# Kernel tuning notes

Measured on AMD Instinct MI355X. Metric: run time of the kernel, lower is better.

## Reference

```python
import jax, jax.numpy as jnp
import numpy as np

N, E, IN_F, EDGE_F, HID, S = 200000, 600000, 28, 4, 128, 20000
NUM_LAYERS = 4
L = NUM_LAYERS - 1
BN_EPS = 1e-5


def setup_inputs() -> dict:
    key = jax.random.key(0)
    ks = jax.random.split(key, 20)
    p = lambda k, shape: (jax.random.normal(k, shape, dtype=jnp.float32) * 0.1)
    return {
        'x': jax.random.normal(ks[0], (N, IN_F), dtype=jnp.float32),
        'edge_index': jax.random.randint(ks[1], (2, E), 0, N),
        'edge_attr': jax.random.normal(ks[2], (E, EDGE_F), dtype=jnp.float32),
        'edge_weight': jax.random.uniform(ks[3], (E,), dtype=jnp.float32),
        'node_mask': (jax.random.uniform(ks[4], (N,)) > 0.5).astype(jnp.float32),
        'subgraphs2nodes': jax.random.randint(ks[5], (N,), 0, S),
        # layer-1 params (in_features -> hidden)
        'be1_W1': p(ks[6], (EDGE_F, IN_F)), 'be1_b1': jnp.zeros((IN_F,), jnp.float32),
        'be1_W2': p(ks[7], (IN_F, IN_F)), 'be1_b2': jnp.zeros((IN_F,), jnp.float32),
        'm1_W1': p(ks[8], (IN_F, HID)), 'm1_b1': jnp.zeros((HID,), jnp.float32),
        'm1_W2': p(ks[9], (HID, HID)), 'm1_b2': jnp.zeros((HID,), jnp.float32),
        'bn1_g': jnp.ones((HID,), jnp.float32), 'bn1_b': jnp.zeros((HID,), jnp.float32),
        'eps1': jnp.zeros((), jnp.float32),
        # layers 2..NUM_LAYERS, stacked (hidden -> hidden)
        'beW1': p(ks[10], (L, EDGE_F, HID)), 'beb1': jnp.zeros((L, HID), jnp.float32),
        'beW2': p(ks[11], (L, HID, HID)), 'beb2': jnp.zeros((L, HID), jnp.float32),
        'mW1': p(ks[12], (L, HID, HID)), 'mb1': jnp.zeros((L, HID), jnp.float32),
        'mW2': p(ks[13], (L, HID, HID)), 'mb2': jnp.zeros((L, HID), jnp.float32),
        'bng': jnp.ones((L, HID), jnp.float32), 'bnb': jnp.zeros((L, HID), jnp.float32),
        'eps': jnp.zeros((L,), jnp.float32),
    }


def _mlp2(h, W1, b1, W2, b2):
    # Linear -> ReLU -> Linear
    return jnp.dot(jax.nn.relu(jnp.dot(h, W1) + b1), W2) + b2


def _gine(x, src, dst, edge_attr, edge_weight, eps,
          beW1, beb1, beW2, beb2, W1, b1, W2, b2, g, beta):
    # bond encoder on edge features
    e = _mlp2(edge_attr, beW1, beb1, beW2, beb2)            # [E, d]
    # message: relu(x_j + e_ij) * w_ij, aggregated at dst via scatter-add
    m = jax.nn.relu(x[src] + e) * edge_weight[:, None]      # [E, d]
    aggr = jax.ops.segment_sum(m, dst, num_segments=N)      # [N, d]
    h = (1.0 + eps) * x + aggr
    # node MLP: Linear,ReLU,Linear,BN(train mode),ReLU
    h = _mlp2(h, W1, b1, W2, b2)
    mu = jnp.mean(h, axis=0)
    var = jnp.mean((h - mu) ** 2, axis=0)
    h = (h - mu) * jax.lax.rsqrt(var + BN_EPS) * g + beta
    return jax.nn.relu(h)


def reference(x, edge_index, edge_attr, edge_weight, node_mask, subgraphs2nodes,
              be1_W1, be1_b1, be1_W2, be1_b2, m1_W1, m1_b1, m1_W2, m1_b2,
              bn1_g, bn1_b, eps1,
              beW1, beb1, beW2, beb2, mW1, mb1, mW2, mb2, bng, bnb, eps):
    src, dst = edge_index[0], edge_index[1]
    h = _gine(x, src, dst, edge_attr, edge_weight, eps1,
              be1_W1, be1_b1, be1_W2, be1_b2,
              m1_W1, m1_b1, m1_W2, m1_b2, bn1_g, bn1_b)
    for i in range(L):
        h_new = _gine(h, src, dst, edge_attr, edge_weight, eps[i],
                      beW1[i], beb1[i], beW2[i], beb2[i],
                      mW1[i], mb1[i], mW2[i], mb2[i], bng[i], bnb[i])
        h = h + h_new  # residual
    # float node_mask branch + global_add_pool over subgraphs2nodes
    h = h * node_mask[:, None]
    return jax.ops.segment_sum(h, subgraphs2nodes, num_segments=S)  # [S, HID]
```

## Files before the change

### kernel.cpp

```cpp
#include <hip/hip_runtime.h>
#include <hip/hip_bf16.h>


#define BNEPS 1e-5f
#define LDA 136
#define SCAN_NB 240

typedef __attribute__((ext_vector_type(8))) short bf16x8;
typedef __attribute__((ext_vector_type(8))) unsigned short u16x8;
typedef __attribute__((ext_vector_type(4))) float f32x4;

__device__ inline short f2bf(float f) {
    __hip_bfloat16 h = __float2bfloat16(f);
    return *reinterpret_cast<short*>(&h);
}
__device__ inline unsigned short f2bfu(float f) {
    __hip_bfloat16 h = __float2bfloat16(f);
    return *reinterpret_cast<unsigned short*>(&h);
}
__device__ inline float bf2f(unsigned short u) {
    union { unsigned int i; float f; } v; v.i = ((unsigned int)u) << 16; return v.f;
}


__global__ __launch_bounds__(256) void k_prep(
    const float* __restrict__ m1W2, const float* __restrict__ beW2,
    const float* __restrict__ mW1, const float* __restrict__ mW2,
    short* __restrict__ out)
{
    __shared__ float tileS[64][65];
    int b = blockIdx.x, mat = b >> 2, t = b & 3;
    const float* Wsrc;
    if (mat == 0) Wsrc = m1W2;
    else {
        int l = (mat - 1) / 3, which = (mat - 1) % 3;
        Wsrc = (which == 0) ? beW2 + (size_t)l * 16384
             : (which == 1) ? mW1 + (size_t)l * 16384
             :                mW2 + (size_t)l * 16384;
    }
    short* dst = out + (size_t)mat * 16384;
    int tr = (t >> 1) * 64, tc = (t & 1) * 64;
    for (int i = threadIdx.x; i < 4096; i += 256) {
        int r = i >> 6, c = i & 63;
        tileS[r][c] = Wsrc[(size_t)(tr + r) * 128 + (tc + c)];
    }
    __syncthreads();
    for (int i = threadIdx.x; i < 4096; i += 256) {
        int kl = i & 63, nl = i >> 6;
        int n = tc + nl, k = tr + kl;
        int fo = (((n >> 4) * 4 + (k >> 5)) * 64 + (((k >> 3) & 3) * 16 + (n & 15))) * 8 + (k & 7);
        dst[fo] = f2bf(tileS[kl][nl]);
    }
}

__global__ __launch_bounds__(256) void k_prep1(
    const float* __restrict__ W1, short* __restrict__ out)
{
    for (int i = threadIdx.x; i < 4096; i += 256) {
        int j = i & 7, sub = (i >> 3) & 63, nt = i >> 9;
        int quad = sub >> 4, l15 = sub & 15;
        int n = nt * 16 + l15, k = quad * 8 + j;
        out[i] = (k < 28) ? f2bf(W1[(size_t)k * 128 + n]) : (short)0;
    }
}

__global__ __launch_bounds__(256) void k_prep28(
    const float* __restrict__ W2, short* __restrict__ out)
{
    for (int i = threadIdx.x; i < 32 * 32; i += 256) {
        int n = i >> 5, k = i & 31;
        out[i] = (n < 28 && k < 28) ? f2bf(W2[(size_t)k * 28 + n]) : (short)0;
    }
}

__global__ __launch_bounds__(256) void k_prepx(
    const float* __restrict__ x, unsigned short* __restrict__ xbf, int N)
{
    int total = N * 32;
    for (int i = blockIdx.x * 256 + threadIdx.x; i < total; i += gridDim.x * 256) {
        int n = i >> 5, c = i & 31;
        xbf[i] = (c < 28) ? f2bfu(x[(size_t)n * 28 + c]) : (unsigned short)0;
    }
}

__global__ __launch_bounds__(256) void k_count(
    const int* __restrict__ ei, int* __restrict__ counts, int E)
{
    for (int e = blockIdx.x * 256 + threadIdx.x; e < E; e += gridDim.x * 256)
        atomicAdd(&counts[ei[E + e]], 1);
}

__global__ __launch_bounds__(256) void k_count2(
    const int* __restrict__ s2n, const float* __restrict__ mask,
    int* __restrict__ counts2, int N)
{
    for (int n = blockIdx.x * 256 + threadIdx.x; n < N; n += gridDim.x * 256)
        if (mask[n] != 0.f) atomicAdd(&counts2[s2n[n]], 1);
}

__global__ __launch_bounds__(256) void k_scanA(
    const int* __restrict__ counts, int* __restrict__ bsum, int N, int seg)
{
    __shared__ int red[256];
    int b = blockIdx.x;
    int lo = b * seg, hi = min(lo + seg, N);
    int s = 0;
    for (int i = lo + threadIdx.x; i < hi; i += 256) s += counts[i];
    red[threadIdx.x] = s;
    __syncthreads();
    for (int d = 128; d > 0; d >>= 1) {
        if (threadIdx.x < d) red[threadIdx.x] += red[threadIdx.x + d];
        __syncthreads();
    }
    if (threadIdx.x == 0) bsum[b] = red[0];
}

__global__ __launch_bounds__(256) void k_scanB(
    int* __restrict__ bsum, int nb, int* __restrict__ offs, int N)
{
    __shared__ int sh[256];
    int v = (threadIdx.x < nb) ? bsum[threadIdx.x] : 0;
    sh[threadIdx.x] = v;
    __syncthreads();
    for (int d = 1; d < 256; d <<= 1) {
        int t = (threadIdx.x >= d) ? sh[threadIdx.x - d] : 0;
        __syncthreads();
        sh[threadIdx.x] += t;
        __syncthreads();
    }
    if (threadIdx.x < nb) bsum[threadIdx.x] = sh[threadIdx.x] - v;
    if (threadIdx.x == 0) offs[N] = sh[255];
}

__global__ __launch_bounds__(256) void k_scanC(
    const int* __restrict__ counts, const int* __restrict__ bsum,
    int* __restrict__ offs, int* __restrict__ cursor, int N, int seg)
{
    __shared__ int sh[256];
    int b = blockIdx.x;
    int lo = b * seg, hi = min(lo + seg, N);
    int base = bsum[b];
    for (int t0 = lo; t0 < hi; t0 += 256) {
        int i = t0 + threadIdx.x;
        int v = (i < hi) ? counts[i] : 0;
        sh[threadIdx.x] = v;
        __syncthreads();
        for (int d = 1; d < 256; d <<= 1) {
            int t = (threadIdx.x >= d) ? sh[threadIdx.x - d] : 0;
            __syncthreads();
            sh[threadIdx.x] += t;
            __syncthreads();
        }
        int excl = base + sh[threadIdx.x] - v;
        if (i < hi) { offs[i] = excl; cursor[i] = excl; }
        int tileTotal = sh[255];
        __syncthreads();
        base += tileTotal;
    }
}

__global__ __launch_bounds__(256) void k_scatter(
    const int* __restrict__ ei, const float* __restrict__ ew,
    const float4* __restrict__ ea4,
    int* __restrict__ cursor, int2* __restrict__ pmeta,
    float4* __restrict__ pea4, int E)
{
    for (int e = blockIdx.x * 256 + threadIdx.x; e < E; e += gridDim.x * 256) {
        int d = ei[E + e];
        int pos = atomicAdd(&cursor[d], 1);
        pmeta[pos] = make_int2(ei[e], __float_as_int(ew[e]));
        pea4[pos] = ea4[e];
    }
}

__global__ __launch_bounds__(256) void k_scatter2(
    const int* __restrict__ s2n, const float* __restrict__ mask,
    int* __restrict__ cursor2, int* __restrict__ perm2, int N)
{
    for (int n = blockIdx.x * 256 + threadIdx.x; n < N; n += gridDim.x * 256)
        if (mask[n] != 0.f) {
            int pos = atomicAdd(&cursor2[s2n[n]], 1);
            perm2[pos] = n;
        }
}

__global__ __launch_bounds__(256, 3) void k_emsg(
    const float4* __restrict__ pea4,
    const float* __restrict__ W1, const float* __restrict__ b1,
    const short* __restrict__ W2f, const float* __restrict__ b2,
    unsigned short* __restrict__ emsg, const int* __restrict__ offs,
    int n0, int n1)
{
    __shared__ short As[64 * LDA];
    __shared__ short Bs[16384];
    int e0 = offs[n0], e1 = offs[n1];
    int tid = threadIdx.x;
    int w = tid >> 6, lane = tid & 63;
    int l15 = lane & 15, quad = lane >> 4;
    int rb = w * 16;
    for (int i = tid; i < 2048; i += 256)
        *(bf16x8*)&Bs[i * 8] = *(const bf16x8*)&W2f[i * 8];
    int c2 = lane * 2;
    float w1a[4], w1b[4];
    #pragma unroll
    for (int a = 0; a < 4; ++a) { w1a[a] = W1[a * 128 + c2]; w1b[a] = W1[a * 128 + c2 + 1]; }
    float b1a = b1[c2], b1b = b1[c2 + 1];
    float b2r[8];
    #pragma unroll
    for (int nt = 0; nt < 8; ++nt) b2r[nt] = b2[nt * 16 + l15];
    __syncthreads();

    const float* peaf = (const float*)pea4;
    int numTiles = (e1 - e0 + 63) >> 6;
    for (int tile = blockIdx.x; tile < numTiles; tile += gridDim.x) {
        int base = e0 + tile * 64;
        int eidx = base + rb + (lane >> 2);
        float v = (eidx < e1) ? peaf[(size_t)(base + rb) * 4 + lane] : 0.f;
        #pragma unroll
        for (int e = 0; e < 16; ++e) {
            float a0v = __shfl(v, e * 4 + 0);
            float a1v = __shfl(v, e * 4 + 1);
            float a2v = __shfl(v, e * 4 + 2);
            float a3v = __shfl(v, e * 4 + 3);
            float t0 = fmaf(a0v, w1a[0], fmaf(a1v, w1a[1], fmaf(a2v, w1a[2], fmaf(a3v, w1a[3], b1a))));
            float t1 = fmaf(a0v, w1b[0], fmaf(a1v, w1b[1], fmaf(a2v, w1b[2], fmaf(a3v, w1b[3], b1b))));
            unsigned int pk = ((unsigned int)f2bfu(fmaxf(t1, 0.f)) << 16) | f2bfu(fmaxf(t0, 0.f));
            *(unsigned int*)&As[(rb + e) * LDA + c2] = pk;
        }
        f32x4 acc[8];
        #pragma unroll
        for (int nt = 0; nt < 8; ++nt) acc[nt] = (f32x4){0.f, 0.f, 0.f, 0.f};
        #pragma unroll
        for (int kt = 0; kt < 4; ++kt) {
            bf16x8 af = *(bf16x8*)&As[(rb + l15) * LDA + kt * 32 + quad * 8];
            #pragma unroll
            for (int nt = 0; nt < 8; ++nt) {
                bf16x8 bf = *(const bf16x8*)&Bs[((nt * 4 + kt) * 64 + lane) * 8];
                acc[nt] = __builtin_amdgcn_mfma_f32_16x16x32_bf16(af, bf, acc[nt], 0, 0, 0);
            }
        }
        #pragma unroll
        for (int nt = 0; nt < 8; ++nt) {
            #pragma unroll
            for (int r = 0; r < 4; ++r)
                As[(rb + quad * 4 + r) * LDA + nt * 16 + l15] = f2bf(acc[nt][r] + b2r[nt]);
        }
        #pragma unroll
        for (int it = 0; it < 4; ++it) {
            int arow = rb + it * 4 + quad;
            int gr = base + arow;
            if (gr < e1)
                *(bf16x8*)&emsg[(size_t)(gr - e0) * 128 + l15 * 8] = *(bf16x8*)&As[arow * LDA + l15 * 8];
        }
    }
}

__global__ __launch_bounds__(256) void k_emsg28_mm(
    const float4* __restrict__ pea4,
    const float* __restrict__ W1, const float* __restrict__ b1,
    const short* __restrict__ W2t28,
    const float* __restrict__ b2,
    unsigned short* __restrict__ emsg28, int E)
{
    __shared__ short Bs[32 * 40];
    __shared__ short As[64 * 40];
    __shared__ float eas[64][4];
    __shared__ float b2s[32];
    int tid = threadIdx.x;
    for (int i = tid; i < 32 * 32; i += 256) {
        int n = i >> 5, k = i & 31;
        Bs[n * 40 + k] = W2t28[i];
    }
    if (tid < 32) b2s[tid] = (tid < 28) ? b2[tid] : 0.f;
    int j = tid & 31, sub = tid >> 5;
    float w10 = 0.f, w11 = 0.f, w12 = 0.f, w13 = 0.f, b1j = 0.f;
    if (j < 28) { w10 = W1[j]; w11 = W1[28 + j]; w12 = W1[56 + j]; w13 = W1[84 + j]; b1j = b1[j]; }
    int w = tid >> 6, lane = tid & 63;
    int l15 = lane & 15, quad = lane >> 4;
    __syncthreads();

    int numTiles = (E + 63) >> 6;
    for (int tile = blockIdx.x; tile < numTiles; tile += gridDim.x) {
        int base = tile * 64;
        __syncthreads();
        if (tid < 64) {
            int k = base + tid;
            float4 a = (k < E) ? pea4[k] : make_float4(0.f, 0.f, 0.f, 0.f);
            eas[tid][0] = a.x; eas[tid][1] = a.y; eas[tid][2] = a.z; eas[tid][3] = a.w;
        }
        __syncthreads();
        #pragma unroll
        for (int q = 0; q < 8; ++q) {
            int e = q * 8 + sub;
            float t = fmaf(eas[e][0], w10, fmaf(eas[e][1], w11,
                      fmaf(eas[e][2], w12, fmaf(eas[e][3], w13, b1j))));
            As[e * 40 + j] = (j < 28) ? f2bf(fmaxf(t, 0.f)) : (short)0;
        }
        __syncthreads();
        f32x4 acc[2];
        acc[0] = (f32x4){0.f, 0.f, 0.f, 0.f};
        acc[1] = (f32x4){0.f, 0.f, 0.f, 0.f};
        bf16x8 af = *(bf16x8*)&As[(w * 16 + l15) * 40 + quad * 8];
        #pragma unroll
        for (int nt = 0; nt < 2; ++nt) {
            bf16x8 bf = *(bf16x8*)&Bs[(nt * 16 + l15) * 40 + quad * 8];
            acc[nt] = __builtin_amdgcn_mfma_f32_16x16x32_bf16(af, bf, acc[nt], 0, 0, 0);
        }
        __syncthreads();
        #pragma unroll
        for (int nt = 0; nt < 2; ++nt) {
            int col = nt * 16 + l15;
            float bb = b2s[col];
            #pragma unroll
            for (int r = 0; r < 4; ++r)
                As[(w * 16 + quad * 4 + r) * 40 + col] = f2bf(acc[nt][r] + bb);
        }
        __syncthreads();
        for (int i = tid; i < 64 * 28; i += 256) {
            int row = i / 28, col = i - row * 28;
            int gr = base + row;
            if (gr < E) emsg28[(size_t)gr * 28 + col] = As[row * 40 + col];
        }
    }
}

__global__ __launch_bounds__(256) void k_gather(
    const unsigned short* __restrict__ h, const int* __restrict__ offs,
    const int2* __restrict__ pmeta, const unsigned short* __restrict__ emsg,
    unsigned short* __restrict__ a0,
    const float* __restrict__ epsp, int epsIdx,
    int n0, int n1)
{
    int grp = threadIdx.x >> 5, lane = threadIdx.x & 31;
    int n = n0 + blockIdx.x * 8 + grp;
    if (n >= n1) return;
    int e0 = offs[n0];
    int k0 = offs[n], k1 = offs[n + 1];
    float s = 1.0f + epsp[epsIdx];
    ushort4 hv0 = *(const ushort4*)&h[(size_t)n * 128 + lane * 4];
    float m0 = s * bf2f(hv0.x), m1 = s * bf2f(hv0.y);
    float m2 = s * bf2f(hv0.z), m3 = s * bf2f(hv0.w);
    int2 mtA = make_int2(0, 0), mtB = make_int2(0, 0);
    int2 mtC = make_int2(0, 0), mtD = make_int2(0, 0);
    ushort4 evA = {0,0,0,0}, hvA = {0,0,0,0}, evB = {0,0,0,0}, hvB = {0,0,0,0};
    ushort4 evC = {0,0,0,0}, hvC = {0,0,0,0}, evD = {0,0,0,0}, hvD = {0,0,0,0};
    #define GLOADSLOT(mt, ev, hv, kk) \
        if ((kk) < k1) { \
            mt = pmeta[kk]; \
            ev = *(const ushort4*)&emsg[(size_t)((kk) - e0) * 128 + lane * 4]; \
            hv = *(const ushort4*)&h[(size_t)mt.x * 128 + lane * 4]; \
        }
    GLOADSLOT(mtA, evA, hvA, k0)
    GLOADSLOT(mtB, evB, hvB, k0 + 1)
    GLOADSLOT(mtC, evC, hvC, k0 + 2)
    GLOADSLOT(mtD, evD, hvD, k0 + 3)
    for (int k = k0; k < k1; ++k) {
        float w = __int_as_float(mtA.y);
        m0 += fmaxf(bf2f(hvA.x) + bf2f(evA.x), 0.f) * w;
        m1 += fmaxf(bf2f(hvA.y) + bf2f(evA.y), 0.f) * w;
        m2 += fmaxf(bf2f(hvA.z) + bf2f(evA.z), 0.f) * w;
        m3 += fmaxf(bf2f(hvA.w) + bf2f(evA.w), 0.f) * w;
        mtA = mtB; evA = evB; hvA = hvB;
        mtB = mtC; evB = evC; hvB = hvC;
        mtC = mtD; evC = evD; hvC = hvD;
        GLOADSLOT(mtD, evD, hvD, k + 4)
    }
    #undef GLOADSLOT
    ushort4 o;
    o.x = f2bfu(m0); o.y = f2bfu(m1); o.z = f2bfu(m2); o.w = f2bfu(m3);
    *(ushort4*)&a0[(size_t)n * 128 + lane * 4] = o;
}

__global__ __launch_bounds__(256) void k_gather28(
    const float* __restrict__ x, const unsigned short* __restrict__ xbf,
    const int* __restrict__ offs,
    const int2* __restrict__ pmeta, const unsigned short* __restrict__ emsg28,
    const float* __restrict__ eps1, float* __restrict__ u28, int N)
{
    int grp = threadIdx.x >> 5, lane = threadIdx.x & 31;
    int n = blockIdx.x * 8 + grp;
    if (n >= N || lane >= 28) return;
    float s = 1.0f + eps1[0];
    int k0 = offs[n], k1 = offs[n + 1];
    float m = 0.f;
    int2 mtA = make_int2(0, 0), mtB = make_int2(0, 0);
    int2 mtC = make_int2(0, 0), mtD = make_int2(0, 0);
    unsigned short eA = 0, xA = 0, eB = 0, xB = 0;
    unsigned short eC = 0, xC = 0, eD = 0, xD = 0;
    #define GLOADSLOT28(mt, ee, xx, kk) \
        if ((kk) < k1) { \
            mt = pmeta[kk]; \
            ee = emsg28[(size_t)(kk) * 28 + lane]; \
            xx = xbf[(size_t)mt.x * 32 + lane]; \
        }
    GLOADSLOT28(mtA, eA, xA, k0)
    GLOADSLOT28(mtB, eB, xB, k0 + 1)
    GLOADSLOT28(mtC, eC, xC, k0 + 2)
    GLOADSLOT28(mtD, eD, xD, k0 + 3)
    for (int k = k0; k < k1; ++k) {
        float w = __int_as_float(mtA.y);
        m += fmaxf(bf2f(xA) + bf2f(eA), 0.f) * w;
        mtA = mtB; eA = eB; xA = xB;
        mtB = mtC; eB = eC; xB = xC;
        mtC = mtD; eC = eD; xC = xD;
        GLOADSLOT28(mtD, eD, xD, k + 4)
    }
    #undef GLOADSLOT28
    u28[(size_t)n * 28 + lane] = fmaf(s, x[(size_t)n * 28 + lane], m);
}

__global__ __launch_bounds__(512, 2) void k_mlp(
    const unsigned short* __restrict__ src, const short* __restrict__ W1f,
    const float* __restrict__ b1, const short* __restrict__ W2f,
    const float* __restrict__ b2, unsigned short* __restrict__ dst,
    float* __restrict__ stats, int N)
{
    __shared__ short As[256 * LDA];
    __shared__ short Bs1[16384];
    __shared__ short Bs2[16384];
    __shared__ float sstat[256];
    int tid = threadIdx.x;
    for (int i = tid; i < 2048; i += 512) {
        *(bf16x8*)&Bs1[i * 8] = *(const bf16x8*)&W1f[i * 8];
        *(bf16x8*)&Bs2[i * 8] = *(const bf16x8*)&W2f[i * 8];
    }
    if (tid < 256) sstat[tid] = 0.f;
    int w = tid >> 6, lane = tid & 63;
    int l15 = lane & 15, quad = lane >> 4;
    int rb = w * 32;
    float b1r[8], b2r[8], lsum[8], lsq[8];
    #pragma unroll
    for (int nt = 0; nt < 8; ++nt) {
        b1r[nt] = b1[nt * 16 + l15]; b2r[nt] = b2[nt * 16 + l15];
        lsum[nt] = 0.f; lsq[nt] = 0.f;
    }
    int numTiles = (N + 255) >> 8;
    bf16x8 st[8];
    {
        int tile = blockIdx.x;
        if (tile < numTiles) {
            int base = tile * 256;
            #pragma unroll
            for (int kk = 0; kk < 8; ++kk) {
                int i = tid + kk * 512;
                int rr = base + (i >> 4);
                st[kk] = (rr < N) ? *(const bf16x8*)&src[(size_t)rr * 128 + (i & 15) * 8]
                                  : (bf16x8){0, 0, 0, 0, 0, 0, 0, 0};
            }
        }
    }
    __syncthreads();

    for (int tile = blockIdx.x; tile < numTiles; tile += gridDim.x) {
        int base = tile * 256;
        #pragma unroll
        for (int kk = 0; kk < 8; ++kk) {
            int i = tid + kk * 512;
            *(bf16x8*)&As[(i >> 4) * LDA + (i & 15) * 8] = st[kk];
        }
        int tnext = tile + gridDim.x;
        if (tnext < numTiles) {
            int bn = tnext * 256;
            #pragma unroll
            for (int kk = 0; kk < 8; ++kk) {
                int i = tid + kk * 512;
                int rr = bn + (i >> 4);
                st[kk] = (rr < N) ? *(const bf16x8*)&src[(size_t)rr * 128 + (i & 15) * 8]
                                  : (bf16x8){0, 0, 0, 0, 0, 0, 0, 0};
            }
        }
        __syncthreads();
        f32x4 acc[2][8];
        #pragma unroll
        for (int rg = 0; rg < 2; ++rg)
            #pragma unroll
            for (int nt = 0; nt < 8; ++nt) acc[rg][nt] = (f32x4){0.f, 0.f, 0.f, 0.f};
        #pragma unroll
        for (int kt = 0; kt < 4; ++kt) {
            bf16x8 af0 = *(bf16x8*)&As[(rb + l15) * LDA + kt * 32 + quad * 8];
            bf16x8 af1 = *(bf16x8*)&As[(rb + 16 + l15) * LDA + kt * 32 + quad * 8];
            #pragma unroll
            for (int nt = 0; nt < 8; ++nt) {
                bf16x8 bf = *(const bf16x8*)&Bs1[((nt * 4 + kt) * 64 + lane) * 8];
                acc[0][nt] = __builtin_amdgcn_mfma_f32_16x16x32_bf16(af0, bf, acc[0][nt], 0, 0, 0);
                acc[1][nt] = __builtin_amdgcn_mfma_f32_16x16x32_bf16(af1, bf, acc[1][nt], 0, 0, 0);
            }
        }
        #pragma unroll
        for (int rg = 0; rg < 2; ++rg)
            #pragma unroll
            for (int nt = 0; nt < 8; ++nt)
                #pragma unroll
                for (int r = 0; r < 4; ++r)
                    As[(rb + rg * 16 + quad * 4 + r) * LDA + nt * 16 + l15] =
                        f2bf(fmaxf(acc[rg][nt][r] + b1r[nt], 0.f));
        #pragma unroll
        for (int rg = 0; rg < 2; ++rg)
            #pragma unroll
            for (int nt = 0; nt < 8; ++nt) acc[rg][nt] = (f32x4){0.f, 0.f, 0.f, 0.f};
        #pragma unroll
        for (int kt = 0; kt < 4; ++kt) {
            bf16x8 af0 = *(bf16x8*)&As[(rb + l15) * LDA + kt * 32 + quad * 8];
            bf16x8 af1 = *(bf16x8*)&As[(rb + 16 + l15) * LDA + kt * 32 + quad * 8];
            #pragma unroll
            for (int nt = 0; nt < 8; ++nt) {
                bf16x8 bf = *(const bf16x8*)&Bs2[((nt * 4 + kt) * 64 + lane) * 8];
                acc[0][nt] = __builtin_amdgcn_mfma_f32_16x16x32_bf16(af0, bf, acc[0][nt], 0, 0, 0);
                acc[1][nt] = __builtin_amdgcn_mfma_f32_16x16x32_bf16(af1, bf, acc[1][nt], 0, 0, 0);
            }
        }
        #pragma unroll
        for (int rg = 0; rg < 2; ++rg)
            #pragma unroll
            for (int nt = 0; nt < 8; ++nt) {
                int row0 = base + rb + rg * 16 + quad * 4;
                #pragma unroll
                for (int r = 0; r < 4; ++r) {
                    float z = acc[rg][nt][r] + b2r[nt];
                    if (row0 + r < N) { lsum[nt] += z; lsq[nt] = fmaf(z, z, lsq[nt]); }
                    As[(rb + rg * 16 + quad * 4 + r) * LDA + nt * 16 + l15] = f2bf(z);
                }
            }
        #pragma unroll
        for (int it = 0; it < 8; ++it) {
            int arow = rb + it * 4 + quad;
            int rr = base + arow;
            if (rr < N)
                *(bf16x8*)&dst[(size_t)rr * 128 + l15 * 8] = *(bf16x8*)&As[arow * LDA + l15 * 8];
        }
        __syncthreads();
    }
    #pragma unroll
    for (int nt = 0; nt < 8; ++nt) {
        atomicAdd(&sstat[nt * 16 + l15], lsum[nt]);
        atomicAdd(&sstat[128 + nt * 16 + l15], lsq[nt]);
    }
    __syncthreads();
    if (tid < 256) atomicAdd(&stats[tid], sstat[tid]);
}

__global__ __launch_bounds__(512, 2) void k_mlp1(
    const float* __restrict__ u28, const short* __restrict__ W1f,
    const float* __restrict__ b1, const short* __restrict__ W2f,
    const float* __restrict__ b2, unsigned short* __restrict__ dst,
    float* __restrict__ stats, int N)
{
    __shared__ short A28[256 * 40];
    __shared__ short As[256 * LDA];
    __shared__ short Bs1[4096];
    __shared__ short Bs2[16384];
    __shared__ float sstat[256];
    int tid = threadIdx.x;
    if (tid < 512) {
        int i = tid;
        *(bf16x8*)&Bs1[i * 8] = *(const bf16x8*)&W1f[i * 8];
    }
    for (int i = tid; i < 2048; i += 512)
        *(bf16x8*)&Bs2[i * 8] = *(const bf16x8*)&W2f[i * 8];
    for (int i = tid; i < 1024; i += 512) {
        int row = i >> 2, c = 28 + (i & 3);
        A28[row * 40 + c] = 0;
    }
    if (tid < 256) sstat[tid] = 0.f;
    int w = tid >> 6, lane = tid & 63;
    int l15 = lane & 15, quad = lane >> 4;
    int rb = w * 32;
    float b1r[8], b2r[8], lsum[8], lsq[8];
    #pragma unroll
    for (int nt = 0; nt < 8; ++nt) {
        b1r[nt] = b1[nt * 16 + l15]; b2r[nt] = b2[nt * 16 + l15];
        lsum[nt] = 0.f; lsq[nt] = 0.f;
    }
    int numTiles = (N + 255) >> 8;
    float stf[14];
    {
        int tile = blockIdx.x;
        if (tile < numTiles) {
            int base = tile * 256;
            #pragma unroll
            for (int kk = 0; kk < 14; ++kk) {
                int idx = tid + kk * 512;
                int row = idx / 28, col = idx - row * 28;
                int rr = base + row;
                stf[kk] = (rr < N) ? u28[(size_t)rr * 28 + col] : 0.f;
            }
        }
    }
    __syncthreads();

    for (int tile = blockIdx.x; tile < numTiles; tile += gridDim.x) {
        int base = tile * 256;
        #pragma unroll
        for (int kk = 0; kk < 14; ++kk) {
            int idx = tid + kk * 512;
            int row = idx / 28, col = idx - row * 28;
            A28[row * 40 + col] = f2bf(stf[kk]);
        }
        int tnext = tile + gridDim.x;
        if (tnext < numTiles) {
            int bn = tnext * 256;
            #pragma unroll
            for (int kk = 0; kk < 14; ++kk) {
                int idx = tid + kk * 512;
                int row = idx / 28, col = idx - row * 28;
                int rr = bn + row;
                stf[kk] = (rr < N) ? u28[(size_t)rr * 28 + col] : 0.f;
            }
        }
        __syncthreads();
        f32x4 acc[2][8];
        #pragma unroll
        for (int rg = 0; rg < 2; ++rg)
            #pragma unroll
            for (int nt = 0; nt < 8; ++nt) acc[rg][nt] = (f32x4){0.f, 0.f, 0.f, 0.f};
        {
            bf16x8 af0 = *(bf16x8*)&A28[(rb + l15) * 40 + quad * 8];
            bf16x8 af1 = *(bf16x8*)&A28[(rb + 16 + l15) * 40 + quad * 8];
            #pragma unroll
            for (int nt = 0; nt < 8; ++nt) {
                bf16x8 bf = *(const bf16x8*)&Bs1[(nt * 64 + lane) * 8];
                acc[0][nt] = __builtin_amdgcn_mfma_f32_16x16x32_bf16(af0, bf, acc[0][nt], 0, 0, 0);
                acc[1][nt] = __builtin_amdgcn_mfma_f32_16x16x32_bf16(af1, bf, acc[1][nt], 0, 0, 0);
            }
        }
        #pragma unroll
        for (int rg = 0; rg < 2; ++rg)
            #pragma unroll
            for (int nt = 0; nt < 8; ++nt)
                #pragma unroll
                for (int r = 0; r < 4; ++r)
                    As[(rb + rg * 16 + quad * 4 + r) * LDA + nt * 16 + l15] =
                        f2bf(fmaxf(acc[rg][nt][r] + b1r[nt], 0.f));
        __syncthreads();
        #pragma unroll
        for (int rg = 0; rg < 2; ++rg)
            #pragma unroll
            for (int nt = 0; nt < 8; ++nt) acc[rg][nt] = (f32x4){0.f, 0.f, 0.f, 0.f};
        #pragma unroll
        for (int kt = 0; kt < 4; ++kt) {
            bf16x8 af0 = *(bf16x8*)&As[(rb + l15) * LDA + kt * 32 + quad * 8];
            bf16x8 af1 = *(bf16x8*)&As[(rb + 16 + l15) * LDA + kt * 32 + quad * 8];
            #pragma unroll
            for (int nt = 0; nt < 8; ++nt) {
                bf16x8 bf = *(const bf16x8*)&Bs2[((nt * 4 + kt) * 64 + lane) * 8];
                acc[0][nt] = __builtin_amdgcn_mfma_f32_16x16x32_bf16(af0, bf, acc[0][nt], 0, 0, 0);
                acc[1][nt] = __builtin_amdgcn_mfma_f32_16x16x32_bf16(af1, bf, acc[1][nt], 0, 0, 0);
            }
        }
        #pragma unroll
        for (int rg = 0; rg < 2; ++rg)
            #pragma unroll
            for (int nt = 0; nt < 8; ++nt) {
                int row0 = base + rb + rg * 16 + quad * 4;
                #pragma unroll
                for (int r = 0; r < 4; ++r) {
                    float z = acc[rg][nt][r] + b2r[nt];
                    if (row0 + r < N) { lsum[nt] += z; lsq[nt] = fmaf(z, z, lsq[nt]); }
                    As[(rb + rg * 16 + quad * 4 + r) * LDA + nt * 16 + l15] = f2bf(z);
                }
            }
        #pragma unroll
        for (int it = 0; it < 8; ++it) {
            int arow = rb + it * 4 + quad;
            int rr = base + arow;
            if (rr < N)
                *(bf16x8*)&dst[(size_t)rr * 128 + l15 * 8] = *(bf16x8*)&As[arow * LDA + l15 * 8];
        }
        __syncthreads();
    }
    #pragma unroll
    for (int nt = 0; nt < 8; ++nt) {
        atomicAdd(&sstat[nt * 16 + l15], lsum[nt]);
        atomicAdd(&sstat[128 + nt * 16 + l15], lsq[nt]);
    }
    __syncthreads();
    if (tid < 256) atomicAdd(&stats[tid], sstat[tid]);
}

__global__ __launch_bounds__(256) void k_bn(
    const unsigned short* __restrict__ z, const float* __restrict__ stats,
    const float* __restrict__ g, const float* __restrict__ bb, float invN,
    unsigned short* __restrict__ h, int residual, int N)
{
    __shared__ float ss[256];
    if (threadIdx.x < 128) {
        int j = threadIdx.x;
        float mu  = stats[j] * invN;
        float var = fmaf(stats[128 + j], invN, -mu * mu);
        float sc  = rsqrtf(fmaxf(var, 0.f) + BNEPS) * g[j];
        ss[j] = sc;
        ss[128 + j] = fmaf(-mu, sc, bb[j]);
    }
    __syncthreads();
    int idx8 = blockIdx.x * 256 + threadIdx.x;
    int stride = gridDim.x * 256;
    int c0 = (idx8 & 15) * 8;
    float scl[8], sht[8];
    #pragma unroll
    for (int r = 0; r < 8; ++r) { scl[r] = ss[c0 + r]; sht[r] = ss[128 + c0 + r]; }
    int total8 = N * 16;
    for (; idx8 < total8; idx8 += stride) {
        int n = idx8 >> 4;
        u16x8 z8 = *(const u16x8*)&z[(size_t)n * 128 + c0];
        float hn[8];
        #pragma unroll
        for (int r = 0; r < 8; ++r)
            hn[r] = fmaxf(fmaf(bf2f(z8[r]), scl[r], sht[r]), 0.f);
        if (residual) {
            u16x8 h8 = *(const u16x8*)&h[(size_t)n * 128 + c0];
            #pragma unroll
            for (int r = 0; r < 8; ++r) hn[r] += bf2f(h8[r]);
        }
        u16x8 o;
        #pragma unroll
        for (int r = 0; r < 8; ++r) o[r] = f2bfu(hn[r]);
        *(u16x8*)&h[(size_t)n * 128 + c0] = o;
    }
}

__global__ __launch_bounds__(256) void k_poolbn(
    const unsigned short* __restrict__ z, const unsigned short* __restrict__ hprev,
    const float* __restrict__ stats, const float* __restrict__ g,
    const float* __restrict__ bb, float invN,
    const int* __restrict__ offs2, const int* __restrict__ perm2,
    float* __restrict__ out, int S)
{
    __shared__ float ss[256];
    if (threadIdx.x < 128) {
        int j = threadIdx.x;
        float mu  = stats[j] * invN;
        float var = fmaf(stats[128 + j], invN, -mu * mu);
        float sc  = rsqrtf(fmaxf(var, 0.f) + BNEPS) * g[j];
        ss[j] = sc;
        ss[128 + j] = fmaf(-mu, sc, bb[j]);
    }
    __syncthreads();
    int w = threadIdx.x >> 6, lane = threadIdx.x & 63;
    int s = blockIdx.x * 4 + w;
    if (s >= S) return;
    int c0 = lane * 2;
    float scl0 = ss[c0], scl1 = ss[c0 + 1];
    float sht0 = ss[128 + c0], sht1 = ss[128 + c0 + 1];
    int k0 = offs2[s], k1 = offs2[s + 1];
    float a0 = 0.f, a1 = 0.f;
    for (int k = k0; k < k1; ++k) {
        int n = perm2[k];
        ushort2 zv = *(const ushort2*)&z[(size_t)n * 128 + c0];
        ushort2 hv = *(const ushort2*)&hprev[(size_t)n * 128 + c0];
        a0 += fmaxf(fmaf(bf2f(zv.x), scl0, sht0), 0.f) + bf2f(hv.x);
        a1 += fmaxf(fmaf(bf2f(zv.y), scl1, sht1), 0.f) + bf2f(hv.y);
    }
    *(float2*)&out[(size_t)s * 128 + c0] = make_float2(a0, a1);
}

extern "C" void kernel_launch(void* const* d_in, const int* in_sizes, int n_in,
                              void* d_out, int out_size, void* d_ws, size_t ws_size,
                              hipStream_t stream) {
    const float* x    = (const float*)d_in[0];
    const int*   ei   = (const int*)d_in[1];
    const float* ea   = (const float*)d_in[2];
    const float* ew   = (const float*)d_in[3];
    const float* mask = (const float*)d_in[4];
    const int*   s2n  = (const int*)d_in[5];
    const float* be1W1 = (const float*)d_in[6];
    const float* be1b1 = (const float*)d_in[7];
    const float* be1W2 = (const float*)d_in[8];
    const float* be1b2 = (const float*)d_in[9];
    const float* m1W1  = (const float*)d_in[10];
    const float* m1b1  = (const float*)d_in[11];
    const float* m1W2  = (const float*)d_in[12];
    const float* m1b2  = (const float*)d_in[13];
    const float* bn1g  = (const float*)d_in[14];
    const float* bn1b  = (const float*)d_in[15];
    const float* eps1  = (const float*)d_in[16];
    const float* beW1  = (const float*)d_in[17];
    const float* beb1  = (const float*)d_in[18];
    const float* beW2  = (const float*)d_in[19];
    const float* beb2  = (const float*)d_in[20];
    const float* mW1   = (const float*)d_in[21];
    const float* mb1   = (const float*)d_in[22];
    const float* mW2   = (const float*)d_in[23];
    const float* mb2   = (const float*)d_in[24];
    const float* bng   = (const float*)d_in[25];
    const float* bnb   = (const float*)d_in[26];
    const float* epsL  = (const float*)d_in[27];

    const int N = in_sizes[0] / 28;
    const int E = in_sizes[1] / 2;
    const int S = out_size / 128;
    const float invN = 1.0f / (float)N;
    const int NS = N / 2;
    const int EMC = E / 2 + 8192;

    auto al16 = [](size_t v) { return (v + 15) & ~(size_t)15; };
    char* ws = (char*)d_ws;
    size_t offH      = 0;
    size_t offA0     = al16(offH + (size_t)N * 256);
    size_t offEm     = al16(offA0 + (size_t)N * 256);
    size_t emBytes   = (size_t)EMC * 256;
    if ((size_t)E * 56 > emBytes) emBytes = (size_t)E * 56;
    size_t offStats  = al16(offEm + emBytes);
    size_t offSS     = al16(offStats + 4096);
    size_t offWts    = al16(offSS + 1024);
    size_t offCounts = al16(offWts + 10 * 16384 * 2 + 4096 * 2 + 1024 * 2);
    size_t offOffs   = al16(offCounts + (size_t)N * 4);
    size_t offCursor = al16(offOffs + (size_t)(N + 1) * 4);
    size_t offPmeta  = al16(offCursor + (size_t)N * 4);
    size_t offPea    = al16(offPmeta + (size_t)E * 8);
    size_t offBsum   = al16(offPea + (size_t)E * 16);
    size_t offCnt2   = al16(offBsum + SCAN_NB * 4);
    size_t offOffs2  = al16(offCnt2 + (size_t)S * 4);
    size_t offCur2   = al16(offOffs2 + (size_t)(S + 1) * 4);
    size_t offPerm2  = al16(offCur2 + (size_t)S * 4);
    size_t need      = offPerm2 + (size_t)N * 4;
    if (ws_size < need) return;

    unsigned short* h    = (unsigned short*)(ws + offH);
    unsigned short* a0   = (unsigned short*)(ws + offA0);
    unsigned short* emsg = (unsigned short*)(ws + offEm);
    float* u28    = (float*)(ws + offA0);
    unsigned short* xbf = (unsigned short*)(ws + offA0 + 26214400);
    float* stats  = (float*)(ws + offStats);
    short* wts    = (short*)(ws + offWts);
    short* w1p    = wts + 10 * 16384;
    short* w2p28  = w1p + 4096;
    int*   counts = (int*)(ws + offCounts);
    int*   offs   = (int*)(ws + offOffs);
    int*   cursor = (int*)(ws + offCursor);
    int2*  pmeta  = (int2*)(ws + offPmeta);
    float4* pea4  = (float4*)(ws + offPea);
    int*   bsum   = (int*)(ws + offBsum);
    int*   cnt2   = (int*)(ws + offCnt2);
    int*   offs2  = (int*)(ws + offOffs2);
    int*   cur2   = (int*)(ws + offCur2);
    int*   perm2  = (int*)(ws + offPerm2);
    const float4* ea4 = (const float4*)ea;

    hipMemsetAsync(stats, 0, 4 * 256 * sizeof(float), stream);
    hipMemsetAsync(counts, 0, (size_t)N * sizeof(int), stream);
    hipMemsetAsync(cnt2, 0, (size_t)S * sizeof(int), stream);

    k_prep<<<40, 256, 0, stream>>>(m1W2, beW2, mW1, mW2, wts);
    k_prep1<<<1, 256, 0, stream>>>(m1W1, w1p);
    k_prep28<<<1, 256, 0, stream>>>(be1W2, w2p28);
    k_prepx<<<512, 256, 0, stream>>>(x, xbf, N);

    const int seg = (N + SCAN_NB - 1) / SCAN_NB;
    k_count<<<1024, 256, 0, stream>>>(ei, counts, E);
    k_scanA<<<SCAN_NB, 256, 0, stream>>>(counts, bsum, N, seg);
    k_scanB<<<1, 256, 0, stream>>>(bsum, SCAN_NB, offs, N);
    k_scanC<<<SCAN_NB, 256, 0, stream>>>(counts, bsum, offs, cursor, N, seg);
    k_scatter<<<1024, 256, 0, stream>>>(ei, ew, ea4, cursor, pmeta, pea4, E);

    const int seg2 = (S + SCAN_NB - 1) / SCAN_NB;
    k_count2<<<512, 256, 0, stream>>>(s2n, mask, cnt2, N);
    k_scanA<<<SCAN_NB, 256, 0, stream>>>(cnt2, bsum, S, seg2);
    k_scanB<<<1, 256, 0, stream>>>(bsum, SCAN_NB, offs2, S);
    k_scanC<<<SCAN_NB, 256, 0, stream>>>(cnt2, bsum, offs2, cur2, S, seg2);
    k_scatter2<<<512, 256, 0, stream>>>(s2n, mask, cur2, perm2, N);

    auto wt_be = [&](int l) { return wts + (size_t)(1 + 3 * l + 0) * 16384; };
    auto wt_m1 = [&](int l) { return wts + (size_t)(1 + 3 * l + 1) * 16384; };
    auto wt_m2 = [&](int l) { return wts + (size_t)(1 + 3 * l + 2) * 16384; };

    k_emsg28_mm<<<2048, 256, 0, stream>>>(pea4, be1W1, be1b1, w2p28, be1b2, emsg, E);
    k_gather28<<<(N + 7) / 8, 256, 0, stream>>>(x, xbf, offs, pmeta, emsg, eps1, u28, N);
    k_mlp1<<<256, 512, 0, stream>>>(u28, w1p, m1b1, wts , m1b2, h, stats, N);
    k_bn<<<2048, 256, 0, stream>>>(h, stats, bn1g, bn1b, invN, h, 0, N);

    for (int l = 0; l < 3; ++l) {
        for (int c = 0; c < 2; ++c) {
            int n0 = (c == 0) ? 0 : NS;
            int n1 = (c == 0) ? NS : N;
            k_emsg<<<2048, 256, 0, stream>>>(pea4,
                beW1 + (size_t)l * 512, beb1 + (size_t)l * 128,
                wt_be(l), beb2 + (size_t)l * 128, emsg, offs, n0, n1);
            k_gather<<<(n1 - n0 + 7) / 8, 256, 0, stream>>>(h, offs, pmeta, emsg, a0,
                epsL, l, n0, n1);
        }
        k_mlp<<<256, 512, 0, stream>>>(a0, wt_m1(l), mb1 + (size_t)l * 128,
                                       wt_m2(l), mb2 + (size_t)l * 128, a0,
                                       stats + 256 * (l + 1), N);
        if (l < 2) {
            k_bn<<<2048, 256, 0, stream>>>(a0, stats + 256 * (l + 1),
                bng + (size_t)l * 128, bnb + (size_t)l * 128, invN, h, 1, N);
        }
    }

    k_poolbn<<<(S + 3) / 4, 256, 0, stream>>>(a0, h, stats + 256 * 3,
        bng + 256, bnb + 256, invN, offs2, perm2, (float*)d_out, S);
}
```

Measured before the change: 1.008 ms.

## Fuse message computation into edge-encoder kernels, simplify gather to sum

The edge-encoder kernels now gather the source node features and edge weight themselves and write the finished message relu(h_src + e) * w, rounded to bf16, instead of the raw edge embedding. The gather kernels then just sum the precomputed messages per destination node, with no pmeta or random h loads. This moves the random source-node gather into the edge-parallel kernel, so the segmented gather only streams contiguous emsg rows. The message is now rounded to bf16 before summation, which slightly changes numerics, and the software prefetch pipeline in the gather loops is removed.

```diff
diff --git a/kernel.cpp b/kernel.cpp
--- a/kernel.cpp
+++ b/kernel.cpp
@@ -188,6 +188,7 @@
     const float4* __restrict__ pea4,
     const float* __restrict__ W1, const float* __restrict__ b1,
     const short* __restrict__ W2f, const float* __restrict__ b2,
+    const int2* __restrict__ pmeta, const unsigned short* __restrict__ h,
     unsigned short* __restrict__ emsg, const int* __restrict__ offs,
     int n0, int n1)
 {
@@ -216,6 +217,17 @@
         int base = e0 + tile * 64;
         int eidx = base + rb + (lane >> 2);
         float v = (eidx < e1) ? peaf[(size_t)(base + rb) * 4 + lane] : 0.f;
+        float ws[16];
+        unsigned int hsv[16];
+        #pragma unroll
+        for (int e = 0; e < 16; ++e) {
+            int ge = base + rb + e;
+            if (ge < e1) {
+                int2 mt = pmeta[ge];
+                ws[e] = __int_as_float(mt.y);
+                hsv[e] = *(const unsigned int*)&h[(size_t)mt.x * 128 + c2];
+            } else { ws[e] = 0.f; hsv[e] = 0; }
+        }
         #pragma unroll
         for (int e = 0; e < 16; ++e) {
             float a0v = __shfl(v, e * 4 + 0);
@@ -246,11 +258,16 @@
                 As[(rb + quad * 4 + r) * LDA + nt * 16 + l15] = f2bf(acc[nt][r] + b2r[nt]);
         }
         #pragma unroll
-        for (int it = 0; it < 4; ++it) {
-            int arow = rb + it * 4 + quad;
-            int gr = base + arow;
-            if (gr < e1)
-                *(bf16x8*)&emsg[(size_t)(gr - e0) * 128 + l15 * 8] = *(bf16x8*)&As[arow * LDA + l15 * 8];
+        for (int e = 0; e < 16; ++e) {
+            int gr = base + rb + e;
+            if (gr < e1) {
+                unsigned int zp = *(unsigned int*)&As[(rb + e) * LDA + c2];
+                unsigned int hp = hsv[e];
+                float m0 = fmaxf(bf2f((unsigned short)(hp & 0xffff)) + bf2f((unsigned short)(zp & 0xffff)), 0.f) * ws[e];
+                float m1 = fmaxf(bf2f((unsigned short)(hp >> 16)) + bf2f((unsigned short)(zp >> 16)), 0.f) * ws[e];
+                unsigned int pk = ((unsigned int)f2bfu(m1) << 16) | f2bfu(m0);
+                *(unsigned int*)&emsg[(size_t)(gr - e0) * 128 + c2] = pk;
+            }
         }
     }
 }
@@ -260,6 +277,7 @@
     const float* __restrict__ W1, const float* __restrict__ b1,
     const short* __restrict__ W2t28,
     const float* __restrict__ b2,
+    const int2* __restrict__ pmeta, const unsigned short* __restrict__ xbf,
     unsigned short* __restrict__ emsg28, int E)
 {
     __shared__ short Bs[32 * 40];
@@ -319,14 +337,20 @@
         for (int i = tid; i < 64 * 28; i += 256) {
             int row = i / 28, col = i - row * 28;
             int gr = base + row;
-            if (gr < E) emsg28[(size_t)gr * 28 + col] = As[row * 40 + col];
+            if (gr < E) {
+                int2 mt = pmeta[gr];
+                float xs = bf2f(xbf[(size_t)mt.x * 32 + col]);
+                float z = bf2f((unsigned short)As[row * 40 + col]);
+                float m = fmaxf(xs + z, 0.f) * __int_as_float(mt.y);
+                emsg28[(size_t)gr * 28 + col] = f2bfu(m);
+            }
         }
     }
 }
 
 __global__ __launch_bounds__(256) void k_gather(
     const unsigned short* __restrict__ h, const int* __restrict__ offs,
-    const int2* __restrict__ pmeta, const unsigned short* __restrict__ emsg,
+    const unsigned short* __restrict__ emsg,
     unsigned short* __restrict__ a0,
     const float* __restrict__ epsp, int epsIdx,
     int n0, int n1)
@@ -340,41 +364,28 @@
     ushort4 hv0 = *(const ushort4*)&h[(size_t)n * 128 + lane * 4];
     float m0 = s * bf2f(hv0.x), m1 = s * bf2f(hv0.y);
     float m2 = s * bf2f(hv0.z), m3 = s * bf2f(hv0.w);
-    int2 mtA = make_int2(0, 0), mtB = make_int2(0, 0);
-    int2 mtC = make_int2(0, 0), mtD = make_int2(0, 0);
-    ushort4 evA = {0,0,0,0}, hvA = {0,0,0,0}, evB = {0,0,0,0}, hvB = {0,0,0,0};
-    ushort4 evC = {0,0,0,0}, hvC = {0,0,0,0}, evD = {0,0,0,0}, hvD = {0,0,0,0};
-    #define GLOADSLOT(mt, ev, hv, kk) \
-        if ((kk) < k1) { \
-            mt = pmeta[kk]; \
-            ev = *(const ushort4*)&emsg[(size_t)((kk) - e0) * 128 + lane * 4]; \
-            hv = *(const ushort4*)&h[(size_t)mt.x * 128 + lane * 4]; \
-        }
-    GLOADSLOT(mtA, evA, hvA, k0)
-    GLOADSLOT(mtB, evB, hvB, k0 + 1)
-    GLOADSLOT(mtC, evC, hvC, k0 + 2)
-    GLOADSLOT(mtD, evD, hvD, k0 + 3)
-    for (int k = k0; k < k1; ++k) {
-        float w = __int_as_float(mtA.y);
-        m0 += fmaxf(bf2f(hvA.x) + bf2f(evA.x), 0.f) * w;
-        m1 += fmaxf(bf2f(hvA.y) + bf2f(evA.y), 0.f) * w;
-        m2 += fmaxf(bf2f(hvA.z) + bf2f(evA.z), 0.f) * w;
-        m3 += fmaxf(bf2f(hvA.w) + bf2f(evA.w), 0.f) * w;
-        mtA = mtB; evA = evB; hvA = hvB;
-        mtB = mtC; evB = evC; hvB = hvC;
-        mtC = mtD; evC = evD; hvC = hvD;
-        GLOADSLOT(mtD, evD, hvD, k + 4)
-    }
-    #undef GLOADSLOT
+    int k = k0;
+    for (; k + 1 < k1; k += 2) {
+        ushort4 evA = *(const ushort4*)&emsg[(size_t)(k - e0) * 128 + lane * 4];
+        ushort4 evB = *(const ushort4*)&emsg[(size_t)(k + 1 - e0) * 128 + lane * 4];
+        m0 += bf2f(evA.x) + bf2f(evB.x);
+        m1 += bf2f(evA.y) + bf2f(evB.y);
+        m2 += bf2f(evA.z) + bf2f(evB.z);
+        m3 += bf2f(evA.w) + bf2f(evB.w);
+    }
+    if (k < k1) {
+        ushort4 ev = *(const ushort4*)&emsg[(size_t)(k - e0) * 128 + lane * 4];
+        m0 += bf2f(ev.x); m1 += bf2f(ev.y);
+        m2 += bf2f(ev.z); m3 += bf2f(ev.w);
+    }
     ushort4 o;
     o.x = f2bfu(m0); o.y = f2bfu(m1); o.z = f2bfu(m2); o.w = f2bfu(m3);
     *(ushort4*)&a0[(size_t)n * 128 + lane * 4] = o;
 }
 
 __global__ __launch_bounds__(256) void k_gather28(
-    const float* __restrict__ x, const unsigned short* __restrict__ xbf,
-    const int* __restrict__ offs,
-    const int2* __restrict__ pmeta, const unsigned short* __restrict__ emsg28,
+    const float* __restrict__ x, const int* __restrict__ offs,
+    const unsigned short* __restrict__ emsg28,
     const float* __restrict__ eps1, float* __restrict__ u28, int N)
 {
     int grp = threadIdx.x >> 5, lane = threadIdx.x & 31;
@@ -383,29 +394,13 @@
     float s = 1.0f + eps1[0];
     int k0 = offs[n], k1 = offs[n + 1];
     float m = 0.f;
-    int2 mtA = make_int2(0, 0), mtB = make_int2(0, 0);
-    int2 mtC = make_int2(0, 0), mtD = make_int2(0, 0);
-    unsigned short eA = 0, xA = 0, eB = 0, xB = 0;
-    unsigned short eC = 0, xC = 0, eD = 0, xD = 0;
-    #define GLOADSLOT28(mt, ee, xx, kk) \
-        if ((kk) < k1) { \
-            mt = pmeta[kk]; \
-            ee = emsg28[(size_t)(kk) * 28 + lane]; \
-            xx = xbf[(size_t)mt.x * 32 + lane]; \
-        }
-    GLOADSLOT28(mtA, eA, xA, k0)
-    GLOADSLOT28(mtB, eB, xB, k0 + 1)
-    GLOADSLOT28(mtC, eC, xC, k0 + 2)
-    GLOADSLOT28(mtD, eD, xD, k0 + 3)
-    for (int k = k0; k < k1; ++k) {
-        float w = __int_as_float(mtA.y);
-        m += fmaxf(bf2f(xA) + bf2f(eA), 0.f) * w;
-        mtA = mtB; eA = eB; xA = xB;
-        mtB = mtC; eB = eC; xB = xC;
-        mtC = mtD; eC = eD; xC = xD;
-        GLOADSLOT28(mtD, eD, xD, k + 4)
-    }
-    #undef GLOADSLOT28
+    int k = k0;
+    for (; k + 1 < k1; k += 2) {
+        float eA = bf2f(emsg28[(size_t)k * 28 + lane]);
+        float eB = bf2f(emsg28[(size_t)(k + 1) * 28 + lane]);
+        m += eA + eB;
+    }
+    if (k < k1) m += bf2f(emsg28[(size_t)k * 28 + lane]);
     u28[(size_t)n * 28 + lane] = fmaf(s, x[(size_t)n * 28 + lane], m);
 }
 
@@ -863,8 +858,9 @@
     auto wt_m1 = [&](int l) { return wts + (size_t)(1 + 3 * l + 1) * 16384; };
     auto wt_m2 = [&](int l) { return wts + (size_t)(1 + 3 * l + 2) * 16384; };
 
-    k_emsg28_mm<<<2048, 256, 0, stream>>>(pea4, be1W1, be1b1, w2p28, be1b2, emsg, E);
-    k_gather28<<<(N + 7) / 8, 256, 0, stream>>>(x, xbf, offs, pmeta, emsg, eps1, u28, N);
+    k_emsg28_mm<<<2048, 256, 0, stream>>>(pea4, be1W1, be1b1, w2p28, be1b2,
+                                          pmeta, xbf, emsg, E);
+    k_gather28<<<(N + 7) / 8, 256, 0, stream>>>(x, offs, emsg, eps1, u28, N);
     k_mlp1<<<256, 512, 0, stream>>>(u28, w1p, m1b1, wts , m1b2, h, stats, N);
     k_bn<<<2048, 256, 0, stream>>>(h, stats, bn1g, bn1b, invN, h, 0, N);
 
@@ -874,8 +870,8 @@
             int n1 = (c == 0) ? NS : N;
             k_emsg<<<2048, 256, 0, stream>>>(pea4,
                 beW1 + (size_t)l * 512, beb1 + (size_t)l * 128,
-                wt_be(l), beb2 + (size_t)l * 128, emsg, offs, n0, n1);
-            k_gather<<<(n1 - n0 + 7) / 8, 256, 0, stream>>>(h, offs, pmeta, emsg, a0,
+                wt_be(l), beb2 + (size_t)l * 128, pmeta, h, emsg, offs, n0, n1);
+            k_gather<<<(n1 - n0 + 7) / 8, 256, 0, stream>>>(h, offs, emsg, a0,
                 epsL, l, n0, n1);
         }
         k_mlp<<<256, 512, 0, stream>>>(a0, wt_m1(l), mb1 + (size_t)l * 128,
```

Measured after the change: 1.143 ms. 13.3% more time.
